# Kernel optimization log

Measured on AMD Instinct MI355X. Metric: run time of the kernel, lower is better.

## Reference

```python
import jax, jax.numpy as jnp
import numpy as np

EMBED = 1024
HEADS = 16
HEAD_DIM = EMBED // HEADS


def setup_inputs() -> dict:
    key = jax.random.key(0)
    k1, k2, k3, k4, k5 = jax.random.split(key, 5)
    x = jax.random.normal(k1, (2, 2048, EMBED), dtype=jnp.float32)
    # torch nn.Linear params: weight [out, in], bias [out]; y = x @ W.T + b
    s_attn = 1.0 / np.sqrt(EMBED)
    w_attn = jax.random.uniform(k2, (3 * EMBED, EMBED), jnp.float32, -s_attn, s_attn)
    b_attn = jax.random.uniform(k3, (3 * EMBED,), jnp.float32, -s_attn, s_attn)
    w_proj = jax.random.uniform(k4, (EMBED, EMBED), jnp.float32, -s_attn, s_attn)
    b_proj = jax.random.uniform(k5, (EMBED,), jnp.float32, -s_attn, s_attn)
    return {"x": x, "w_attn": w_attn, "b_attn": b_attn, "w_proj": w_proj, "b_proj": b_proj}


def reference(x, w_attn, b_attn, w_proj, b_proj):
    B, S, D = x.shape
    qkv = x @ w_attn.T + b_attn                      # [B, S, 3D]
    q, k, v = jnp.split(qkv, 3, axis=-1)             # each [B, S, D]

    def heads(t):  # [B, S, D] -> [B, H, S, hd]
        return t.reshape(B, S, HEADS, HEAD_DIM).transpose(0, 2, 1, 3)

    q, k, v = heads(q), heads(k), heads(v)
    # Faithful to source: NO 1/sqrt(d) scaling, NO causal mask.
    w = jnp.einsum('bhqd,bhkd->bhqk', q, k)          # [B, H, S, S]
    w = jax.nn.softmax(w, axis=-1)
    a = jnp.einsum('bhqk,bhkd->bhqd', w, v)          # [B, H, S, hd]
    a = a.transpose(0, 2, 1, 3).reshape(B, S, D)     # merge heads
    return a @ w_proj.T + b_proj
```

## Files before the change

### kernel.cpp

```cpp
#include <hip/hip_runtime.h>
#include <hip/hip_bf16.h>
#include <stdint.h>
#include <math.h>


typedef __attribute__((ext_vector_type(4))) float f32x4;
typedef __attribute__((ext_vector_type(16))) float f32x16;
typedef __attribute__((ext_vector_type(8))) short bf16x8;

static __device__ __forceinline__ unsigned short f2bf(float f) {
    unsigned u = __float_as_uint(f);
    u += 0x7FFFu + ((u >> 16) & 1u);
    return (unsigned short)(u >> 16);
}
static __device__ __forceinline__ unsigned cvt_pk_bf16(float a, float b) {
    unsigned r;
    asm("v_cvt_pk_bf16_f32 %0, %1, %2" : "=v"(r) : "v"(a), "v"(b));
    return r;
}

typedef const __attribute__((address_space(1))) unsigned int* gas_ptr;
typedef __attribute__((address_space(3))) unsigned int* las_ptr;
static __device__ __forceinline__ void gload_lds16(const void* g, void* l) {
    __builtin_amdgcn_global_lo\
ad_lds((gas_ptr)g, (las_ptr)l, 16, 0, 0);
}

__global__ void conv_bf16_kernel(const float* __restrict__ src,
                                 unsigned short* __restrict__ dst, int n4) {
    int i = blockIdx.x * blockDim.x + threadIdx.x;
    int stride = gridDim.x * blockDim.x;
    for (; i < n4; i += stride) {
        float4 v = ((const float4*)src)[i];
        ushort4 o;
        o.x = f2bf(v.x); o.y = f2bf(v.y); o.z = f2bf(v.z); o.w = f2bf(v.w);
        ((ushort4*)dst)[i] = o;
    }
}

template <int MODE>
__global__ __launch_bounds__(256, 2) void gemm_bt_kernel(
    const unsigned short* __restrict__ A,
    const unsigned short* __restrict__ Bw,
    const float* __restrict__ bias,
    unsigned short* __restrict__ q1,
    unsigned short* __restrict__ k1,
    unsigned short* __restrict__ vT,
    float* __restrict__ outp,
    int N, int K)
{
    __shared__ __align__(16) unsigned char lds[32768];
    const int t  = threadIdx.x;
    const int lane = t & 63;
    const int w  = t >> 6;
    const int wr = w >> 1, wc = w & 1;
    const int lg = lane >> 4, ll = lane & 15;
    const int m0 = blockIdx.y * 128;
    const int n0 = blockIdx.x * 128;

    f32x4 acc[4][4] = {};

    const int srow  = t >> 3;
    const int sslot = t & 7;
    const unsigned short* Abase[4];
    const unsigned short* Bbase[4];
#pragma unroll
    for (int ci = 0; ci < 4; ++ci) {
        int r  = ci * 32 + srow;
        int cg = sslot ^ (r & 7);
        Abase[ci] = A  + (size_t)(m0 + r) * K + cg * 8;
        Bbase[ci] = Bw + (size_t)(n0 + r) * K + cg * 8;
    }

    for (int k0 = 0; k0 < K; k0 += 64) {
#pragma unroll
        for (int ci = 0; ci < 4; ++ci)
            gload_lds16(Abase[ci] + k0, lds + ci*4096 + (t>>6)*1024);
#pragma unroll
        for (int ci = 0; ci < 4; ++ci)
            gload_lds16(Bbase[ci] + k0, lds + 16384 + ci*4096 + (t>>6)*1024);
        __syncthreads();

        bf16x8 af[4][2], bfr[4][2];
#pragma unroll
        for (int mt = 0; mt < 4; ++mt)
#pragma unroll
            for (int kc = 0; kc < 2; ++kc) {
                int row = wr*64 + mt*16 + ll;
                int cg  = (4*kc + lg) ^ (row & 7);
                af[mt][kc] = *(const bf16x8*)(lds + row*128 + cg*16);
            }
#pragma unroll
        for (int nt = 0; nt < 4; ++nt)
#pragma unroll
            for (int kc = 0; kc < 2; ++kc) {
                int row = wc*64 + nt*16 + ll;
                int cg  = (4*kc + lg) ^ (row & 7);
                bfr[nt][kc] = *(const bf16x8*)(lds + 16384 + row*128 + cg*16);
            }
#pragma unroll
        for (int kc = 0; kc < 2; ++kc)
#pragma unroll
            for (int mt = 0; mt < 4; ++mt)
#pragma unroll
                for (int nt = 0; nt < 4; ++nt)
                    acc[mt][nt] = __builtin_amdgcn_mfma_f32_16x16x32_bf16(
                        af[mt][kc], bfr[nt][kc], acc[mt][nt], 0, 0, 0);
        __syncthreads();
    }

#pragma unroll
    for (int mt = 0; mt < 4; ++mt)
#pragma unroll
      for (int nt = 0; nt < 4; ++nt)
#pragma unroll
        for (int r = 0; r < 4; ++r) {
            int m = m0 + wr*64 + mt*16 + 4*lg + r;
            int n = n0 + wc*64 + nt*16 + ll;
            float v = acc[mt][nt][r] + bias[n];
            if (MODE == 0) {
                int bb = m >> 11;
                int s  = m & 2047;
                int which = n >> 10;
                int h  = (n >> 6) & 15;
                int d  = n & 63;
                int bh = bb * 16 + h;
                if (which == 2) {
                    vT[((size_t)bh * 64 + d) * 2048 + s] = f2bf(v);
                } else {
                    float vq = (which == 0) ? v * 1.44269504f : v;
                    unsigned short* dp = (which == 0 ? q1 : k1)
                                       + ((size_t)bh * 2048 + s) * 64 + d;
                    *dp = f2bf(vq);
                }
            } else {
                outp[(size_t)m * N + n] = v;
            }
        }
}

__global__ __launch_bounds__(512, 4) void attn_kernel(
    const unsigned short* __restrict__ q1,
    const unsigned short* __restrict__ k1,
    const unsigned short* __restrict__ vT,
    unsigned short* __restrict__ aout)
{
    __shared__ __align__(16) unsigned char lds[65536];
    const int t = threadIdx.x, lane = t & 63, w = t >> 6;
    const int hi = lane >> 5, lq = lane & 31, l7 = lane & 7;
    const int gp = w >> 2, sw = w & 3;
    const int bh = blockIdx.y;
    const int q0 = blockIdx.x * 128 + sw * 32;

    bf16x8 qf[4];
    {
        const unsigned short* qp = q1 + ((size_t)bh*2048 + q0 + lq)*64 + hi*8;
#pragma unroll
        for (int ks = 0; ks < 4; ++ks)
            qf[ks] = *(const bf16x8*)(qp + ks*16);
    }

    f32x16 o[2] = {};
    float lrow = 0.f;

    const int sr = t >> 3, ss = t & 7;
    const int scg = ss ^ (sr & 7);
    const int psr = (sr & 51) | ((sr & 4) << 1) | ((sr & 8) >> 1);
    const unsigned short* Ksrc = k1 + ((size_t)bh*2048 + psr)*64 + scg*8;
    const unsigned short* Vsrc = vT + ((size_t)bh*64 + sr)*2048 + scg*8;
    const int sdst = w*1024;

    gload_lds16(Ksrc,        lds + sdst);
    gload_lds16(Ksrc + 4096, lds + 8192 + sdst);
    gload_lds16(Vsrc,        lds + 32768 + sdst);
    gload_lds16(Vsrc + 64,   lds + 32768 + 8192 + sdst);
    __syncthreads();

    for (int s = 0; s < 16; ++s) {
        const int cbuf = ((s & 1)*2 + gp) * 8192;
        if (s < 15) {
            const int nb = (((s+1) & 1)*2) * 8192;
            const size_t T2 = 2*s + 2;
            gload_lds16(Ksrc + T2*4096,       lds + nb + sdst);
            gload_lds16(Ksrc + (T2+1)*4096,   lds + nb + 8192 + sdst);
            gload_lds16(Vsrc + T2*64,         lds + 32768 + nb + sdst);
            gload_lds16(Vsrc + (T2+1)*64,     lds + 32768 + nb + 8192 + sdst);
        }
        const unsigned char* Kb = lds + cbuf;
        const unsigned char* Vb = lds + 32768 + cbuf;

        f32x16 sacc[2] = {};
#pragma unroll
        for (int jt = 0; jt < 2; ++jt) {
            const unsigned char* kb = Kb + (jt*32 + lq)*128;
#pragma unroll
            for (int ks = 0; ks < 4; ++ks) {
                int g = (2*ks + hi) ^ l7;
                bf16x8 kf = *(const bf16x8*)(kb + g*16);
                sacc[jt] = __builtin_amdgcn_mfma_f32_32x32x16_bf16(
                    kf, qf[ks], sacc[jt], 0, 0, 0);
            }
        }

        float a0 = 0.f, a1 = 0.f, a2 = 0.f, a3 = 0.f;
        bf16x8 pa[4];
#pragma unroll
        for (int jt = 0; jt < 2; ++jt) {
            float ps[16];
#pragma unroll
            for (int c = 0; c < 4; ++c) {
                ps[4*c]   = exp2f(sacc[jt][4*c]);
                ps[4*c+1] = exp2f(sacc[jt][4*c+1]);
                ps[4*c+2] = exp2f(sacc[jt][4*c+2]);
                ps[4*c+3] = exp2f(sacc[jt][4*c+3]);
                a0 += ps[4*c]; a1 += ps[4*c+1]; a2 += ps[4*c+2]; a3 += ps[4*c+3];
            }
            union { unsigned u[4]; bf16x8 v; } pk0, pk1;
#pragma unroll
            for (int c = 0; c < 4; ++c) {
                pk0.u[c] = cvt_pk_bf16(ps[2*c],     ps[2*c + 1]);
                pk1.u[c] = cvt_pk_bf16(ps[8 + 2*c], ps[8 + 2*c + 1]);
            }
            pa[2*jt]     = pk0.v;
            pa[2*jt + 1] = pk1.v;
        }
        float rs = (a0 + a1) + (a2 + a3);
        rs += __shfl_xor(rs, 32);
        lrow += rs;

#pragma unroll
        for (int dh = 0; dh < 2; ++dh) {
            const unsigned char* vb = Vb + (dh*32 + lq)*128;
#pragma unroll
            for (int ks = 0; ks < 4; ++ks) {
                int g = (2*ks + hi) ^ l7;
                bf16x8 vf = *(const bf16x8*)(vb + g*16);
                o[dh] = __builtin_amdgcn_mfma_f32_32x32x16_bf16(
                    pa[ks], vf, o[dh], 0, 0, 0);
            }
        }
        __syncthreads();
    }

    if (gp == 1) {
        unsigned char* p = lds + sw*9216 + lane*144;
#pragma unroll
        for (int dh = 0; dh < 2; ++dh)
#pragma unroll
            for (int c = 0; c < 4; ++c) {
                f32x4 v;
                v[0] = o[dh][4*c]; v[1] = o[dh][4*c+1];
                v[2] = o[dh][4*c+2]; v[3] = o[dh][4*c+3];
                *(f32x4*)(p + dh*64 + c*16) = v;
            }
        *(float*)(lds + 36864 + sw*256 + lane*4) = lrow;
    }
    __syncthreads();
    if (gp == 0) {
        const unsigned char* p = lds + sw*9216 + lane*144;
#pragma unroll
        for (int dh = 0; dh < 2; ++dh)
#pragma unroll
            for (int c = 0; c < 4; ++c) {
                f32x4 v = *(const f32x4*)(p + dh*64 + c*16);
                o[dh][4*c]   += v[0]; o[dh][4*c+1] += v[1];
                o[dh][4*c+2] += v[2]; o[dh][4*c+3] += v[3];
            }
        lrow += *(const float*)(lds + 36864 + sw*256 + lane*4);

        const int bb = bh >> 4, h = bh & 15;
#pragma unroll
        for (int r = 0; r < 16; ++r) {
            int qrow = (r & 3) + 8*(r >> 2) + 4*hi;
            float linv = 1.0f / __shfl(lrow, qrow);
            size_t srow = q0 + qrow;
#pragma unroll
            for (int dh = 0; dh < 2; ++dh) {
                int d = dh*32 + lq;
                aout[((size_t)(bb*2048 + srow)*16 + h)*64 + d] =
                    f2bf(o[dh][r] * linv);
            }
        }
    }
}

extern "C" void kernel_launch(void* const* d_in, const int* in_sizes, int n_in,
                              void* d_out, int out_size, void* d_ws, size_t ws_size,
                              hipStream_t stream) {
    const float* x      = (const float*)d_in[0];
    const float* w_attn = (const float*)d_in[1];
    const float* b_attn = (const float*)d_in[2];
    const float* w_proj = (const float*)d_in[3];
    const float* b_proj = (const float*)d_in[4];
    float* out = (float*)d_out;

    unsigned char* ws = (unsigned char*)d_ws;
    unsigned short* x1  = (unsigned short*)(ws);
    unsigned short* w1a = (unsigned short*)(ws + (size_t)8*1024*1024);
    unsigned short* wpb = (unsigned short*)(ws + (size_t)14*1024*1024);
    unsigned short* q1  = (unsigned short*)(ws + (size_t)16*1024*1024);
    unsigned short* k1  = (unsigned short*)(ws + (size_t)24*1024*1024);
    unsigned short* vT  = (unsigned short*)(ws + (size_t)32*1024*1024);
    unsigned short* ab  = (unsigned short*)(ws + (size_t)40*1024*1024);

    conv_bf16_kernel<<<1024, 256, 0, stream>>>(x, x1, 1048576);
    conv_bf16_kernel<<<768, 256, 0, stream>>>(w_attn, w1a, 786432);
    conv_bf16_kernel<<<256, 256, 0, stream>>>(w_proj, wpb, 262144);

    gemm_bt_kernel<0><<<dim3(24, 32), 256, 0, stream>>>(
        x1, w1a, b_attn, q1, k1, vT, nullptr, 3072, 1024);

    attn_kernel<<<dim3(16, 32), 512, 0, stream>>>(q1, k1, vT, ab);

    gemm_bt_kernel<1><<<dim3(8, 32), 256, 0, stream>>>(
        ab, wpb, b_proj, nullptr, nullptr, nullptr, out, 1024, 1024);
}
```

Measured before the change: 127.8 us.

## Fuse conversions, swizzle block order, restructure attention loop with MFMA row sums

Merges the three fp32-to-bf16 conversion launches into one kernel and remaps GEMM block indices in groups of eight so co-scheduled blocks share operand tiles in cache. The attention kernel moves to a 1D grid that interleaves heads, and its main loop is unrolled by two with fixed LDS fragment pointers and a macro step. Row sums of the softmax numerator are now produced by an MFMA against a ones vector instead of VALU adds and a cross-lane shuffle. This trades extra matrix-core work and register pressure for fewer VALU, shuffle and launch costs.

```diff
diff --git a/kernel.cpp b/kernel.cpp
--- a/kernel.cpp
+++ b/kernel.cpp
@@ -22,19 +22,26 @@
 typedef const __attribute__((address_space(1))) unsigned int* gas_ptr;
 typedef __attribute__((address_space(3))) unsigned int* las_ptr;
 static __device__ __forceinline__ void gload_lds16(const void* g, void* l) {
-    __builtin_amdgcn_global_lo\
-ad_lds((gas_ptr)g, (las_ptr)l, 16, 0, 0);
-}
-
-__global__ void conv_bf16_kernel(const float* __restrict__ src,
-                                 unsigned short* __restrict__ dst, int n4) {
+    __builtin_amdgcn_global_load_lds((gas_ptr)g, (las_ptr)l, 16, 0, 0);
+}
+
+__global__ void conv_all_kernel(const float* __restrict__ x,
+                                const float* __restrict__ wa,
+                                const float* __restrict__ wp,
+                                unsigned short* __restrict__ x1,
+                                unsigned short* __restrict__ w1a,
+                                unsigned short* __restrict__ wpb) {
     int i = blockIdx.x * blockDim.x + threadIdx.x;
     int stride = gridDim.x * blockDim.x;
-    for (; i < n4; i += stride) {
-        float4 v = ((const float4*)src)[i];
+    for (; i < 2097152; i += stride) {
+        const float* s; unsigned short* d; int j;
+        if (i < 1048576)      { s = x;  d = x1;  j = i; }
+        else if (i < 1835008) { s = wa; d = w1a; j = i - 1048576; }
+        else                  { s = wp; d = wpb; j = i - 1835008; }
+        float4 v = ((const float4*)s)[j];
         ushort4 o;
         o.x = f2bf(v.x); o.y = f2bf(v.y); o.z = f2bf(v.z); o.w = f2bf(v.w);
-        ((ushort4*)dst)[i] = o;
+        ((ushort4*)d)[j] = o;
     }
 }
 
@@ -55,8 +62,13 @@
     const int w  = t >> 6;
     const int wr = w >> 1, wc = w & 1;
     const int lg = lane >> 4, ll = lane & 15;
-    const int m0 = blockIdx.y * 128;
-    const int n0 = blockIdx.x * 128;
+
+    const int gx = gridDim.x;
+    const int flat = blockIdx.y * gx + blockIdx.x;
+    const int cpx = (gx * gridDim.y) >> 3;
+    const int swz = (flat & 7) * cpx + (flat >> 3);
+    const int m0 = (swz / gx) * 128;
+    const int n0 = (swz % gx) * 128;
 
     f32x4 acc[4][4] = {};
 
@@ -149,8 +161,11 @@
     const int t = threadIdx.x, lane = t & 63, w = t >> 6;
     const int hi = lane >> 5, lq = lane & 31, l7 = lane & 7;
     const int gp = w >> 2, sw = w & 3;
-    const int bh = blockIdx.y;
-    const int q0 = blockIdx.x * 128 + sw * 32;
+
+    const int D  = blockIdx.x;
+    const int bh = (D & 7) + ((D >> 7) << 3);
+    const int qb = (D >> 3) & 15;
+    const int q0 = qb * 128 + sw * 32;
 
     bf16x8 qf[4];
     {
@@ -160,8 +175,12 @@
             qf[ks] = *(const bf16x8*)(qp + ks*16);
     }
 
-    f32x16 o[2] = {};
-    float lrow = 0.f;
+    f32x16 o0 = {}, o1 = {};
+    f32x16 ld = {};
+    const f32x16 fz = {};
+    bf16x8 onef;
+#pragma unroll
+    for (int j = 0; j < 8; ++j) onef[j] = (short)0x3F80;
 
     const int sr = t >> 3, ss = t & 7;
     const int scg = ss ^ (sr & 7);
@@ -170,116 +189,151 @@
     const unsigned short* Vsrc = vT + ((size_t)bh*64 + sr)*2048 + scg*8;
     const int sdst = w*1024;
 
+    unsigned char* fb0 = lds + gp*8192 + lq*128 + (((0 + hi) ^ l7) << 4);
+    unsigned char* fb1 = lds + gp*8192 + lq*128 + (((2 + hi) ^ l7) << 4);
+    unsigned char* fb2 = lds + gp*8192 + lq*128 + (((4 + hi) ^ l7) << 4);
+    unsigned char* fb3 = lds + gp*8192 + lq*128 + (((6 + hi) ^ l7) << 4);
+
     gload_lds16(Ksrc,        lds + sdst);
     gload_lds16(Ksrc + 4096, lds + 8192 + sdst);
     gload_lds16(Vsrc,        lds + 32768 + sdst);
     gload_lds16(Vsrc + 64,   lds + 32768 + 8192 + sdst);
     __syncthreads();
 
-    for (int s = 0; s < 16; ++s) {
-        const int cbuf = ((s & 1)*2 + gp) * 8192;
-        if (s < 15) {
-            const int nb = (((s+1) & 1)*2) * 8192;
-            const size_t T2 = 2*s + 2;
-            gload_lds16(Ksrc + T2*4096,       lds + nb + sdst);
-            gload_lds16(Ksrc + (T2+1)*4096,   lds + nb + 8192 + sdst);
-            gload_lds16(Vsrc + T2*64,         lds + 32768 + nb + sdst);
-            gload_lds16(Vsrc + (T2+1)*64,     lds + 32768 + nb + 8192 + sdst);
-        }
-        const unsigned char* Kb = lds + cbuf;
-        const unsigned char* Vb = lds + 32768 + cbuf;
-
-        f32x16 sacc[2] = {};
-#pragma unroll
-        for (int jt = 0; jt < 2; ++jt) {
-            const unsigned char* kb = Kb + (jt*32 + lq)*128;
-#pragma unroll
-            for (int ks = 0; ks < 4; ++ks) {
-                int g = (2*ks + hi) ^ l7;
-                bf16x8 kf = *(const bf16x8*)(kb + g*16);
-                sacc[jt] = __builtin_amdgcn_mfma_f32_32x32x16_bf16(
-                    kf, qf[ks], sacc[jt], 0, 0, 0);
+#define ATTN_STEP(PAR)                                                        \
+    {                                                                         \
+        f32x16 s0, s1;                                                        \
+        bf16x8 kf;                                                            \
+        kf = *(const bf16x8*)(fb0 + (PAR)*16384);                             \
+        s0 = __builtin_amdgcn_mfma_f32_32x32x16_bf16(kf, qf[0], fz, 0,0,0);   \
+        kf = *(const bf16x8*)(fb0 + (PAR)*16384 + 4096);                      \
+        s1 = __builtin_amdgcn_mfma_f32_32x32x16_bf16(kf, qf[0], fz, 0,0,0);   \
+        kf = *(const bf16x8*)(fb1 + (PAR)*16384);                             \
+        s0 = __builtin_amdgcn_mfma_f32_32x32x16_bf16(kf, qf[1], s0, 0,0,0);   \
+        kf = *(const bf16x8*)(fb1 + (PAR)*16384 + 4096);                      \
+        s1 = __builtin_amdgcn_mfma_f32_32x32x16_bf16(kf, qf[1], s1, 0,0,0);   \
+        kf = *(const bf16x8*)(fb2 + (PAR)*16384);                             \
+        s0 = __builtin_amdgcn_mfma_f32_32x32x16_bf16(kf, qf[2], s0, 0,0,0);   \
+        kf = *(const bf16x8*)(fb2 + (PAR)*16384 + 4096);                      \
+        s1 = __builtin_amdgcn_mfma_f32_32x32x16_bf16(kf, qf[2], s1, 0,0,0);   \
+        kf = *(const bf16x8*)(fb3 + (PAR)*16384);                             \
+        s0 = __builtin_amdgcn_mfma_f32_32x32x16_bf16(kf, qf[3], s0, 0,0,0);   \
+        kf = *(const bf16x8*)(fb3 + (PAR)*16384 + 4096);                      \
+        s1 = __builtin_amdgcn_mfma_f32_32x32x16_bf16(kf, qf[3], s1, 0,0,0);   \
+        bf16x8 pa0, pa1, pa2, pa3;                                            \
+        {                                                                     \
+            union { unsigned u[4]; bf16x8 v; } a, b, c, d;                    \
+            a.u[0] = cvt_pk_bf16(exp2f(s0[0]),  exp2f(s0[1]));                \
+            a.u[1] = cvt_pk_bf16(exp2f(s0[2]),  exp2f(s0[3]));                \
+            a.u[2] = cvt_pk_bf16(exp2f(s0[4]),  exp2f(s0[5]));                \
+            a.u[3] = cvt_pk_bf16(exp2f(s0[6]),  exp2f(s0[7]));                \
+            b.u[0] = cvt_pk_bf16(exp2f(s0[8]),  exp2f(s0[9]));                \
+            b.u[1] = cvt_pk_bf16(exp2f(s0[10]), exp2f(s0[11]));               \
+            b.u[2] = cvt_pk_bf16(exp2f(s0[12]), exp2f(s0[13]));               \
+            b.u[3] = cvt_pk_bf16(exp2f(s0[14]), exp2f(s0[15]));               \
+            c.u[0] = cvt_pk_bf16(exp2f(s1[0]),  exp2f(s1[1]));                \
+            c.u[1] = cvt_pk_bf16(exp2f(s1[2]),  exp2f(s1[3]));                \
+            c.u[2] = cvt_pk_bf16(exp2f(s1[4]),  exp2f(s1[5]));                \
+            c.u[3] = cvt_pk_bf16(exp2f(s1[6]),  exp2f(s1[7]));                \
+            d.u[0] = cvt_pk_bf16(exp2f(s1[8]),  exp2f(s1[9]));                \
+            d.u[1] = cvt_pk_bf16(exp2f(s1[10]), exp2f(s1[11]));               \
+            d.u[2] = cvt_pk_bf16(exp2f(s1[12]), exp2f(s1[13]));               \
+            d.u[3] = cvt_pk_bf16(exp2f(s1[14]), exp2f(s1[15]));               \
+            pa0 = a.v; pa1 = b.v; pa2 = c.v; pa3 = d.v;                       \
+        }                                                                     \
+        ld = __builtin_amdgcn_mfma_f32_32x32x16_bf16(pa0, onef, ld, 0,0,0);   \
+        ld = __builtin_amdgcn_mfma_f32_32x32x16_bf16(pa1, onef, ld, 0,0,0);   \
+        ld = __builtin_amdgcn_mfma_f32_32x32x16_bf16(pa2, onef, ld, 0,0,0);   \
+        ld = __builtin_amdgcn_mfma_f32_32x32x16_bf16(pa3, onef, ld, 0,0,0);   \
+        bf16x8 vf;                                                            \
+        vf = *(const bf16x8*)(fb0 + (PAR)*16384 + 32768);                     \
+        o0 = __builtin_amdgcn_mfma_f32_32x32x16_bf16(pa0, vf, o0, 0,0,0);     \
+        vf = *(const bf16x8*)(fb0 + (PAR)*16384 + 32768 + 4096);              \
+        o1 = __builtin_amdgcn_mfma_f32_32x32x16_bf16(pa0, vf, o1, 0,0,0);     \
+        vf = *(const bf16x8*)(fb1 + (PAR)*16384 + 32768);                     \
+        o0 = __builtin_amdgcn_mfma_f32_32x32x16_bf16(pa1, vf, o0, 0,0,0);     \
+        vf = *(const bf16x8*)(fb1 + (PAR)*16384 + 32768 + 4096);              \
+        o1 = __builtin_amdgcn_mfma_f32_32x32x16_bf16(pa1, vf, o1, 0,0,0);     \
+        vf = *(const bf16x8*)(fb2 + (PAR)*16384 + 32768);                     \
+        o0 = __builtin_amdgcn_mfma_f32_32x32x16_bf16(pa2, vf, o0, 0,0,0);     \
+        vf = *(const bf16x8*)(fb2 + (PAR)*16384 + 32768 + 4096);              \
+        o1 = __builtin_amdgcn_mfma_f32_32x32x16_bf16(pa2, vf, o1, 0,0,0);     \
+        vf = *(const bf16x8*)(fb3 + (PAR)*16384 + 32768);                     \
+        o0 = __builtin_amdgcn_mfma_f32_32x32x16_bf16(pa3, vf, o0, 0,0,0);     \
+        vf = *(const bf16x8*)(fb3 + (PAR)*16384 + 32768 + 4096);              \
+        o1 = __builtin_amdgcn_mfma_f32_32x32x16_bf16(pa3, vf, o1, 0,0,0);     \
+    }
+
+    for (int sp = 0; sp < 8; ++sp) {
+        {
+            const size_t T = 4*(size_t)sp + 2;
+            gload_lds16(Ksrc + T*4096,        lds + 16384 + sdst);
+            gload_lds16(Ksrc + T*4096 + 4096, lds + 24576 + sdst);
+            gload_lds16(Vsrc + T*64,          lds + 32768 + 16384 + sdst);
+            gload_lds16(Vsrc + T*64 + 64,     lds + 32768 + 24576 + sdst);
+            ATTN_STEP(0)
+            __syncthreads();
+        }
+        {
+            if (sp < 7) {
+                const size_t T = 4*(size_t)sp + 4;
+                gload_lds16(Ksrc + T*4096,        lds + sdst);
+                gload_lds16(Ksrc + T*4096 + 4096, lds + 8192 + sdst);
+                gload_lds16(Vsrc + T*64,          lds + 32768 + sdst);
+                gload_lds16(Vsrc + T*64 + 64,     lds + 32768 + 8192 + sdst);
             }
-        }
-
-        float a0 = 0.f, a1 = 0.f, a2 = 0.f, a3 = 0.f;
-        bf16x8 pa[4];
-#pragma unroll
-        for (int jt = 0; jt < 2; ++jt) {
-            float ps[16];
-#pragma unroll
-            for (int c = 0; c < 4; ++c) {
-                ps[4*c]   = exp2f(sacc[jt][4*c]);
-                ps[4*c+1] = exp2f(sacc[jt][4*c+1]);
-                ps[4*c+2] = exp2f(sacc[jt][4*c+2]);
-                ps[4*c+3] = exp2f(sacc[jt][4*c+3]);
-                a0 += ps[4*c]; a1 += ps[4*c+1]; a2 += ps[4*c+2]; a3 += ps[4*c+3];
-            }
-            union { unsigned u[4]; bf16x8 v; } pk0, pk1;
-#pragma unroll
-            for (int c = 0; c < 4; ++c) {
-                pk0.u[c] = cvt_pk_bf16(ps[2*c],     ps[2*c + 1]);
-                pk1.u[c] = cvt_pk_bf16(ps[8 + 2*c], ps[8 + 2*c + 1]);
-            }
-            pa[2*jt]     = pk0.v;
-            pa[2*jt + 1] = pk1.v;
-        }
-        float rs = (a0 + a1) + (a2 + a3);
-        rs += __shfl_xor(rs, 32);
-        lrow += rs;
-
-#pragma unroll
-        for (int dh = 0; dh < 2; ++dh) {
-            const unsigned char* vb = Vb + (dh*32 + lq)*128;
-#pragma unroll
-            for (int ks = 0; ks < 4; ++ks) {
-                int g = (2*ks + hi) ^ l7;
-                bf16x8 vf = *(const bf16x8*)(vb + g*16);
-                o[dh] = __builtin_amdgcn_mfma_f32_32x32x16_bf16(
-                    pa[ks], vf, o[dh], 0, 0, 0);
-            }
-        }
-        __syncthreads();
-    }
-
+            ATTN_STEP(1)
+            __syncthreads();
+        }
+    }
+#undef ATTN_STEP
+
+    float* mb = (float*)lds;
     if (gp == 1) {
-        unsigned char* p = lds + sw*9216 + lane*144;
-#pragma unroll
-        for (int dh = 0; dh < 2; ++dh)
-#pragma unroll
-            for (int c = 0; c < 4; ++c) {
-                f32x4 v;
-                v[0] = o[dh][4*c]; v[1] = o[dh][4*c+1];
-                v[2] = o[dh][4*c+2]; v[3] = o[dh][4*c+3];
-                *(f32x4*)(p + dh*64 + c*16) = v;
-            }
-        *(float*)(lds + 36864 + sw*256 + lane*4) = lrow;
+        float* p = mb + ((sw << 6) + lane) * 48;
+#pragma unroll
+        for (int c = 0; c < 4; ++c) {
+            f32x4 v = { o0[4*c], o0[4*c+1], o0[4*c+2], o0[4*c+3] };
+            *(f32x4*)(p + 4*c) = v;
+        }
+#pragma unroll
+        for (int c = 0; c < 4; ++c) {
+            f32x4 v = { o1[4*c], o1[4*c+1], o1[4*c+2], o1[4*c+3] };
+            *(f32x4*)(p + 16 + 4*c) = v;
+        }
+#pragma unroll
+        for (int c = 0; c < 4; ++c) {
+            f32x4 v = { ld[4*c], ld[4*c+1], ld[4*c+2], ld[4*c+3] };
+            *(f32x4*)(p + 32 + 4*c) = v;
+        }
     }
     __syncthreads();
     if (gp == 0) {
-        const unsigned char* p = lds + sw*9216 + lane*144;
-#pragma unroll
-        for (int dh = 0; dh < 2; ++dh)
-#pragma unroll
-            for (int c = 0; c < 4; ++c) {
-                f32x4 v = *(const f32x4*)(p + dh*64 + c*16);
-                o[dh][4*c]   += v[0]; o[dh][4*c+1] += v[1];
-                o[dh][4*c+2] += v[2]; o[dh][4*c+3] += v[3];
-            }
-        lrow += *(const float*)(lds + 36864 + sw*256 + lane*4);
+        const float* p = mb + ((sw << 6) + lane) * 48;
+#pragma unroll
+        for (int c = 0; c < 4; ++c) {
+            f32x4 v = *(const f32x4*)(p + 4*c);
+            o0[4*c] += v[0]; o0[4*c+1] += v[1]; o0[4*c+2] += v[2]; o0[4*c+3] += v[3];
+        }
+#pragma unroll
+        for (int c = 0; c < 4; ++c) {
+            f32x4 v = *(const f32x4*)(p + 16 + 4*c);
+            o1[4*c] += v[0]; o1[4*c+1] += v[1]; o1[4*c+2] += v[2]; o1[4*c+3] += v[3];
+        }
+#pragma unroll
+        for (int c = 0; c < 4; ++c) {
+            f32x4 v = *(const f32x4*)(p + 32 + 4*c);
+            ld[4*c] += v[0]; ld[4*c+1] += v[1]; ld[4*c+2] += v[2]; ld[4*c+3] += v[3];
+        }
 
         const int bb = bh >> 4, h = bh & 15;
 #pragma unroll
         for (int r = 0; r < 16; ++r) {
             int qrow = (r & 3) + 8*(r >> 2) + 4*hi;
-            float linv = 1.0f / __shfl(lrow, qrow);
+            float linv = 1.0f / ld[r];
             size_t srow = q0 + qrow;
-#pragma unroll
-            for (int dh = 0; dh < 2; ++dh) {
-                int d = dh*32 + lq;
-                aout[((size_t)(bb*2048 + srow)*16 + h)*64 + d] =
-                    f2bf(o[dh][r] * linv);
-            }
+            aout[((size_t)(bb*2048 + srow)*16 + h)*64 + lq]      = f2bf(o0[r] * linv);
+            aout[((size_t)(bb*2048 + srow)*16 + h)*64 + 32 + lq] = f2bf(o1[r] * linv);
         }
     }
 }
@@ -303,14 +357,12 @@
     unsigned short* vT  = (unsigned short*)(ws + (size_t)32*1024*1024);
     unsigned short* ab  = (unsigned short*)(ws + (size_t)40*1024*1024);
 
-    conv_bf16_kernel<<<1024, 256, 0, stream>>>(x, x1, 1048576);
-    conv_bf16_kernel<<<768, 256, 0, stream>>>(w_attn, w1a, 786432);
-    conv_bf16_kernel<<<256, 256, 0, stream>>>(w_proj, wpb, 262144);
+    conv_all_kernel<<<2048, 256, 0, stream>>>(x, w_attn, w_proj, x1, w1a, wpb);
 
     gemm_bt_kernel<0><<<dim3(24, 32), 256, 0, stream>>>(
         x1, w1a, b_attn, q1, k1, vT, nullptr, 3072, 1024);
 
-    attn_kernel<<<dim3(16, 32), 512, 0, stream>>>(q1, k1, vT, ab);
+    attn_kernel<<<512, 512, 0, stream>>>(q1, k1, vT, ab);
 
     gemm_bt_kernel<1><<<dim3(8, 32), 256, 0, stream>>>(
         ab, wpb, b_proj, nullptr, nullptr, nullptr, out, 1024, 1024);
```

Result: faster. 125.3 us (-2.0%).
